# Optimization experiments

Hardware: AMD Instinct MI355X
Metric: run time of the kernel (lower is better)

## Reference

```python
import jax, jax.numpy as jnp
import numpy as np

N, L, H, V = 64, 512, 1024, 32000


def setup_inputs() -> dict:
    key = jax.random.key(0)
    k1, k2, k3, k4, k5, k6 = jax.random.split(key, 6)
    s = 1.0 / np.sqrt(H)
    return {
        "x": jax.random.randint(k1, (N, L), 0, V, dtype=jnp.int32),
        "emb": jax.random.normal(k2, (V, H), dtype=jnp.float32) * 0.02,
        "W_hh_w": jax.random.normal(k3, (H, H), dtype=jnp.float32) * s,
        "W_hh_b": jax.random.normal(k4, (H,), dtype=jnp.float32) * s,
        "W_xh_w": jax.random.normal(k5, (H, H), dtype=jnp.float32) * s,
        "W_xh_b": jax.random.normal(k6, (H,), dtype=jnp.float32) * s,
    }


def reference(x, emb, W_hh_w, W_hh_b, W_xh_w, W_xh_b):
    # h_t = tanh(W_hh h_{t-1} + b_hh + W_xh e_t + b_xh); returns (N, L, H)
    now = emb[x]                                    # (N, L, H) embedding lookup
    # W_xh part has no recurrence: precompute for all steps at once.
    xh = jnp.einsum("nlh,oh->nlo", now, W_xh_w) + W_xh_b + W_hh_b  # (N, L, H)

    def step(h, xh_t):
        h = jnp.tanh(h @ W_hh_w.T + xh_t)           # (N, H)
        return h, h

    h0 = jnp.zeros((x.shape[0], W_hh_w.shape[0]), dtype=emb.dtype)
    _, memories = jax.lax.scan(step, h0, jnp.swapaxes(xh, 0, 1))  # (L, N, H)
    return jnp.swapaxes(memories, 0, 1)             # (N, L, H)
```

## Files before the change

kernel.cpp:

```cpp
#include <hip/hip_runtime.h>
#include <math.h>

typedef _Float16 half8 __attribute__((ext_vector_type(8)));
typedef _Float16 half4 __attribute__((ext_vector_type(4)));
typedef float floatx4 __attribute__((ext_vector_type(4)));
typedef float floatx2 __attribute__((ext_vector_type(2)));
typedef unsigned int uintx4 __attribute__((ext_vector_type(4)));

#define NB 64
#define LQ 512
#define HD 1024
#define SENT 0x7E7E7E7Eu

__device__ inline half8 cvt2(const float4 a, const float4 b) {
  half8 h;
  h[0]=(_Float16)a.x; h[1]=(_Float16)a.y; h[2]=(_Float16)a.z; h[3]=(_Float16)a.w;
  h[4]=(_Float16)b.x; h[5]=(_Float16)b.y; h[6]=(_Float16)b.z; h[7]=(_Float16)b.w;
  return h;
}

__device__ inline floatx4 ld_sys16(const void* p) {
  floatx4 r;
  asm volatile("global_load_dwordx4 %0, %1, off sc0 sc1"
               : "=v"(r) : "v"(p) : "memory");
  return r;
}
__device__ inline void st_sys8x2(void* p, floatx2 a, floatx2 b) {
  asm volatile("global_store_dwordx2 %0, %1, off sc0 sc1\n\t"
               "global_store_dwordx2 %0, %2, off offset:512 sc0 sc1"
               :: "v"(p), "v"(a), "v"(b) : "memory");
}
__device__ inline void st_sys4(void* p, unsigned v) {
  asm volatile("global_store_dword %0, %1, off sc0 sc1"
               :: "v"(p), "v"(v) : "memory");
}
__device__ inline void vmcnt0() { asm volatile("s_waitcnt vmcnt(0)" ::: "memory"); }

__device__ inline float ftanh(float x) {
  float e = __expf(2.0f * x);
  return 1.0f - 2.0f / (e + 1.0f);
}

__global__ __launch_bounds__(256) void gemm1_kernel(
    const int* __restrict__ x, const float* __restrict__ emb,
    const float* __restrict__ Wxh, const float* __restrict__ bxh,
    const float* __restrict__ bhh, float* __restrict__ out,
    char* __restrict__ hb)
{
  {
    const int bid = blockIdx.y * gridDim.x + blockIdx.x;
    if (threadIdx.x < 64)
      st_sys4((unsigned*)hb + (size_t)bid * 64 + threadIdx.x, SENT);
  }

  __shared__ alignas(16) _Float16 As[128][72];
  __shared__ alignas(16) _Float16 Bs[128][72];
  const int tid  = threadIdx.x;
  const int lane = tid & 63, wv = tid >> 6;
  const int wm = wv & 1, wn = wv >> 1;
  const int Mbase = blockIdx.x * 128;
  const int Nbase = blockIdx.y * 128;

  const int srow  = tid >> 1;
  const int shalf = tid & 1;
  const size_t erow = (size_t)x[Mbase + srow] * HD;
  const size_t brow = (size_t)(Nbase + srow) * HD;

  floatx4 acc[4][4];
#pragma unroll
  for (int i = 0; i < 4; i++)
#pragma unroll
    for (int j = 0; j < 4; j++) acc[i][j] = (floatx4)0.f;

  for (int c = 0; c < 16; ++c) {
    const int k0 = c * 64 + shalf * 32;
    const float4* ap = (const float4*)(emb + erow + k0);
    const float4* bp = (const float4*)(Wxh + brow + k0);
    float4 av[8], bv[8];
#pragma unroll
    for (int i = 0; i < 8; i++) { av[i] = ap[i]; bv[i] = bp[i]; }
    __syncthreads();
#pragma unroll
    for (int i = 0; i < 4; i++) {
      *(half8*)&As[srow][shalf*32 + i*8] = cvt2(av[2*i], av[2*i+1]);
      *(half8*)&Bs[srow][shalf*32 + i*8] = cvt2(bv[2*i], bv[2*i+1]);
    }
    __syncthreads();
#pragma unroll
    for (int s = 0; s < 2; ++s) {
      const int koff = s*32 + (lane >> 4) * 8;
      half8 af[4], bf[4];
#pragma unroll
      for (int i = 0; i < 4; i++) {
        af[i] = *(const half8*)&As[wm*64 + i*16 + (lane & 15)][koff];
        bf[i] = *(const half8*)&Bs[wn*64 + i*16 + (lane & 15)][koff];
      }
#pragma unroll
      for (int i = 0; i < 4; i++)
#pragma unroll
        for (int j = 0; j < 4; j++)
          acc[i][j] = __builtin_amdgcn_mfma_f32_16x16x32_f16(af[i], bf[j], acc[i][j], 0, 0, 0);
    }
  }
#pragma unroll
  for (int j = 0; j < 4; j++) {
    const int o = Nbase + wn*64 + j*16 + (lane & 15);
    const float bias = bxh[o] + bhh[o];
#pragma unroll
    for (int i = 0; i < 4; i++) {
      const int mb = Mbase + wm*64 + i*16 + ((lane >> 4) * 4);
#pragma unroll
      for (int r = 0; r < 4; r++)
        out[(size_t)(mb + r) * HD + o] = acc[i][j][r] + bias;
    }
  }
}

__global__ __launch_bounds__(256, 1) void rnn_kernel(
    const float* __restrict__ Whh, float* __restrict__ out,
    char* __restrict__ hb)
{
  __shared__ alignas(16) _Float16 Ws[32 * 1024];
  const int tid = threadIdx.x, lane = tid & 63, w = tid >> 6;
  const int j = blockIdx.x, obase = j * 32;
  const int col = lane & 15, quad = lane >> 4;

  {
    const int o = tid >> 3, t8 = tid & 7;
    const float* src = Whh + (size_t)(obase + o) * HD;
#pragma unroll
    for (int i = 0; i < 16; ++i) {
      const int c16 = t8 * 16 + i;
      float4 v0 = *(const float4*)(src + c16 * 8);
      float4 v1 = *(const float4*)(src + c16 * 8 + 4);
      *(half8*)&Ws[o * 1024 + ((c16 ^ (o & 7)) * 8)] = cvt2(v0, v1);
    }
  }
  __syncthreads();

  const int n = 16 * w + col;
  float* outp = out + (size_t)n * LQ * HD + obase + quad * 4;
  char* hbw = hb + (size_t)w * 32768 + (size_t)lane * 16;
  char* pubb = hb + (size_t)w * 32768 + (size_t)j * 1024 +
               (size_t)((quad >> 1) * 256 + col * 16 + (quad & 1) * 8);
  const floatx2 sent2 = __builtin_bit_cast(floatx2, (unsigned long long)SENT << 32 | SENT);

  for (int t = 0; t < LQ; ++t) {
    const float* xp = outp + (size_t)t * HD;
    floatx4 xv0 = *(const floatx4*)xp;
    floatx4 xv1 = *(const floatx4*)(xp + 16);
    floatx4 acc0 = (floatx4)0.f, acc1 = (floatx4)0.f;

    if (t > 0) {
      const char* blk = hbw + (size_t)((t - 1) & 3) * 131072;
      floatx4 hv[32];
      unsigned need = 0xFFFFFFFFu;
      int sweeps = 0;
      do {
#pragma unroll
        for (int c = 0; c < 32; ++c)
          if (need & (1u << c)) hv[c] = ld_sys16(blk + c * 1024);
        vmcnt0();
        __builtin_amdgcn_sched_barrier(0);
#pragma unroll
        for (int c = 0; c < 32; ++c)
          if (need & (1u << c)) {
            uintx4 u = __builtin_bit_cast(uintx4, hv[c]);
            if ((u[0] != SENT) & (u[1] != SENT) & (u[2] != SENT) & (u[3] != SENT))
              need &= ~(1u << c);
          }
      } while (need != 0 && ++sweeps < 4096);

      floatx4 a0a = (floatx4)0.f, a1a = (floatx4)0.f;
      floatx4 a0b = (floatx4)0.f, a1b = (floatx4)0.f;
#pragma unroll
      for (int c = 0; c < 32; ++c) {
        const int sw = ((4 * c + quad) ^ (col & 7)) * 8;
        half8 b0 = *(const half8*)&Ws[col * 1024 + sw];
        half8 b1 = *(const half8*)&Ws[(16 + col) * 1024 + sw];
        half8 hf = __builtin_bit_cast(half8, hv[c]);
        if (c & 1) {
          a0b = __builtin_amdgcn_mfma_f32_16x16x32_f16(b0, hf, a0b, 0, 0, 0);
          a1b = __builtin_amdgcn_mfma_f32_16x16x32_f16(b1, hf, a1b, 0, 0, 0);
        } else {
          a0a = __builtin_amdgcn_mfma_f32_16x16x32_f16(b0, hf, a0a, 0, 0, 0);
          a1a = __builtin_amdgcn_mfma_f32_16x16x32_f16(b1, hf, a1a, 0, 0, 0);
        }
      }
      acc0 = a0a + a0b;
      acc1 = a1a + a1b;
    }

    floatx4 h0, h1;
    half4 p0, p1;
#pragma unroll
    for (int r = 0; r < 4; ++r) {
      h0[r] = ftanh(acc0[r] + xv0[r]);
      h1[r] = ftanh(acc1[r] + xv1[r]);
      p0[r] = (_Float16)h0[r];
      p1[r] = (_Float16)h1[r];
    }

    st_sys8x2(pubb + (size_t)(t & 3) * 131072,
              __builtin_bit_cast(floatx2, p0), __builtin_bit_cast(floatx2, p1));

    st_sys8x2(pubb + (size_t)((t + 2) & 3) * 131072, sent2, sent2);

    float* op = outp + (size_t)t * HD;
    *(floatx4*)op = h0;
    *(floatx4*)(op + 16) = h1;
  }
}

extern "C" void kernel_launch(void* const* d_in, const int* in_sizes, int n_in,
                              void* d_out, int out_size, void* d_ws, size_t ws_size,
                              hipStream_t stream) {
  const int*   x   = (const int*)d_in[0];
  const float* emb = (const float*)d_in[1];
  const float* Whh = (const float*)d_in[2];
  const float* bhh = (const float*)d_in[3];
  const float* Wxh = (const float*)d_in[4];
  const float* bxh = (const float*)d_in[5];
  float* out = (float*)d_out;

  char* hbuf = (char*)d_ws;

  gemm1_kernel<<<dim3(256, 8), 256, 0, stream>>>(x, emb, Wxh, bxh, bhh, out, hbuf);
  rnn_kernel<<<dim3(32), 256, 0, stream>>>(Whh, out, hbuf);
}
```

Baseline: 3.725 ms.

## Halve RNN blocks to 64 outputs each and consume hidden chunks as they arrive

The recurrent kernel now runs 16 blocks instead of 32, each holding 64 rows of W_hh in LDS (128 KB) and publishing two 1 KB hidden-state chunks per step. The aim is to cut the number of producers each step must wait on, which should shrink cross-block sync skew. The poll loop also runs MFMAs on each chunk as soon as the whole wave sees it valid, instead of waiting for all 32 chunks first. In exchange, each block does twice the matrix work per step on fewer compute units, and the serial compute per step grows.

```diff
diff --git a/kernel.cpp b/kernel.cpp
--- a/kernel.cpp
+++ b/kernel.cpp
@@ -120,17 +120,17 @@
     const float* __restrict__ Whh, float* __restrict__ out,
     char* __restrict__ hb)
 {
-  __shared__ alignas(16) _Float16 Ws[32 * 1024];
+  __shared__ alignas(16) _Float16 Ws[64 * 1024];
   const int tid = threadIdx.x, lane = tid & 63, w = tid >> 6;
-  const int j = blockIdx.x, obase = j * 32;
+  const int j = blockIdx.x, obase = j * 64;
   const int col = lane & 15, quad = lane >> 4;
 
   {
-    const int o = tid >> 3, t8 = tid & 7;
+    const int o = tid >> 2, t4 = tid & 3;
     const float* src = Whh + (size_t)(obase + o) * HD;
 #pragma unroll
-    for (int i = 0; i < 16; ++i) {
-      const int c16 = t8 * 16 + i;
+    for (int i = 0; i < 32; ++i) {
+      const int c16 = t4 * 32 + i;
       float4 v0 = *(const float4*)(src + c16 * 8);
       float4 v1 = *(const float4*)(src + c16 * 8 + 4);
       *(half8*)&Ws[o * 1024 + ((c16 ^ (o & 7)) * 8)] = cvt2(v0, v1);
@@ -141,15 +141,20 @@
   const int n = 16 * w + col;
   float* outp = out + (size_t)n * LQ * HD + obase + quad * 4;
   char* hbw = hb + (size_t)w * 32768 + (size_t)lane * 16;
-  char* pubb = hb + (size_t)w * 32768 + (size_t)j * 1024 +
-               (size_t)((quad >> 1) * 256 + col * 16 + (quad & 1) * 8);
+  const size_t off0 = (size_t)((quad >> 1) * 256 + col * 16 + (quad & 1) * 8);
+  char* pub0 = hb + (size_t)w * 32768 + (size_t)(2 * j) * 1024 + off0;
+  char* pub1 = hb + (size_t)w * 32768 + (size_t)(2 * j + 1) * 1024 + off0;
   const floatx2 sent2 = __builtin_bit_cast(floatx2, (unsigned long long)SENT << 32 | SENT);
 
   for (int t = 0; t < LQ; ++t) {
     const float* xp = outp + (size_t)t * HD;
-    floatx4 xv0 = *(const floatx4*)xp;
-    floatx4 xv1 = *(const floatx4*)(xp + 16);
-    floatx4 acc0 = (floatx4)0.f, acc1 = (floatx4)0.f;
+    floatx4 xv[4];
+#pragma unroll
+    for (int g = 0; g < 4; ++g) xv[g] = *(const floatx4*)(xp + g * 16);
+
+    floatx4 acc[4];
+#pragma unroll
+    for (int g = 0; g < 4; ++g) acc[g] = (floatx4)0.f;
 
     if (t > 0) {
       const char* blk = hbw + (size_t)((t - 1) & 3) * 131072;
@@ -166,49 +171,45 @@
         for (int c = 0; c < 32; ++c)
           if (need & (1u << c)) {
             uintx4 u = __builtin_bit_cast(uintx4, hv[c]);
-            if ((u[0] != SENT) & (u[1] != SENT) & (u[2] != SENT) & (u[3] != SENT))
+            const bool ok = __all((u[0] != SENT) & (u[1] != SENT) &
+                                  (u[2] != SENT) & (u[3] != SENT));
+            if (ok) {
               need &= ~(1u << c);
+              const int sw = ((4 * c + quad) ^ (col & 7)) * 8;
+              half8 hf = __builtin_bit_cast(half8, hv[c]);
+#pragma unroll
+              for (int g = 0; g < 4; ++g) {
+                half8 bg = *(const half8*)&Ws[(g * 16 + col) * 1024 + sw];
+                acc[g] = __builtin_amdgcn_mfma_f32_16x16x32_f16(bg, hf, acc[g], 0, 0, 0);
+              }
+            }
           }
       } while (need != 0 && ++sweeps < 4096);
-
-      floatx4 a0a = (floatx4)0.f, a1a = (floatx4)0.f;
-      floatx4 a0b = (floatx4)0.f, a1b = (floatx4)0.f;
-#pragma unroll
-      for (int c = 0; c < 32; ++c) {
-        const int sw = ((4 * c + quad) ^ (col & 7)) * 8;
-        half8 b0 = *(const half8*)&Ws[col * 1024 + sw];
-        half8 b1 = *(const half8*)&Ws[(16 + col) * 1024 + sw];
-        half8 hf = __builtin_bit_cast(half8, hv[c]);
-        if (c & 1) {
-          a0b = __builtin_amdgcn_mfma_f32_16x16x32_f16(b0, hf, a0b, 0, 0, 0);
-          a1b = __builtin_amdgcn_mfma_f32_16x16x32_f16(b1, hf, a1b, 0, 0, 0);
-        } else {
-          a0a = __builtin_amdgcn_mfma_f32_16x16x32_f16(b0, hf, a0a, 0, 0, 0);
-          a1a = __builtin_amdgcn_mfma_f32_16x16x32_f16(b1, hf, a1a, 0, 0, 0);
-        }
+    }
+
+    floatx4 h[4];
+    half4 p[4];
+#pragma unroll
+    for (int g = 0; g < 4; ++g)
+#pragma unroll
+      for (int r = 0; r < 4; ++r) {
+        h[g][r] = ftanh(acc[g][r] + xv[g][r]);
+        p[g][r] = (_Float16)h[g][r];
       }
-      acc0 = a0a + a0b;
-      acc1 = a1a + a1b;
-    }
-
-    floatx4 h0, h1;
-    half4 p0, p1;
-#pragma unroll
-    for (int r = 0; r < 4; ++r) {
-      h0[r] = ftanh(acc0[r] + xv0[r]);
-      h1[r] = ftanh(acc1[r] + xv1[r]);
-      p0[r] = (_Float16)h0[r];
-      p1[r] = (_Float16)h1[r];
-    }
-
-    st_sys8x2(pubb + (size_t)(t & 3) * 131072,
-              __builtin_bit_cast(floatx2, p0), __builtin_bit_cast(floatx2, p1));
-
-    st_sys8x2(pubb + (size_t)((t + 2) & 3) * 131072, sent2, sent2);
+
+    const size_t slot = (size_t)(t & 3) * 131072;
+    st_sys8x2(pub0 + slot, __builtin_bit_cast(floatx2, p[0]),
+                           __builtin_bit_cast(floatx2, p[1]));
+    st_sys8x2(pub1 + slot, __builtin_bit_cast(floatx2, p[2]),
+                           __builtin_bit_cast(floatx2, p[3]));
+
+    const size_t slot2 = (size_t)((t + 2) & 3) * 131072;
+    st_sys8x2(pub0 + slot2, sent2, sent2);
+    st_sys8x2(pub1 + slot2, sent2, sent2);
 
     float* op = outp + (size_t)t * HD;
-    *(floatx4*)op = h0;
-    *(floatx4*)(op + 16) = h1;
+#pragma unroll
+    for (int g = 0; g < 4; ++g) *(floatx4*)(op + g * 16) = h[g];
   }
 }
 
@@ -226,5 +227,5 @@
   char* hbuf = (char*)d_ws;
 
   gemm1_kernel<<<dim3(256, 8), 256, 0, stream>>>(x, emb, Wxh, bxh, bhh, out, hbuf);
-  rnn_kernel<<<dim3(32), 256, 0, stream>>>(Whh, out, hbuf);
-}
+  rnn_kernel<<<dim3(16), 256, 0, stream>>>(Whh, out, hbuf);
+}
```

Result: slower. 5.354 ms (+43.7%).
